# Performance work log

Hardware: AMD Instinct MI355X
Metric: run time of the kernel (lower is better)

Reference implementation:

```python
import jax, jax.numpy as jnp
import numpy as np

A_CUBIC = -0.75  # torch grid_sample bicubic convolution coefficient
INTERP_FACTOR = 0.25
WINDOW = 20
STEP = 4


def _cubic_interp_1d(signal):
    # Replicates torch bicubic grid_sample (align_corners=True, border padding)
    # on a (B,1,1,n) tensor, which reduces to 1D cubic convolution (A=-0.75).
    B, n = signal.shape
    num_points = int((n - 1) / INTERP_FACTOR) + 1
    pos = jnp.linspace(0.0, n - 1, num_points)  # sample positions in index space
    i0 = jnp.floor(pos).astype(jnp.int32)
    s = (pos - i0).astype(signal.dtype)  # frac in [0,1)
    A = A_CUBIC
    def w_far(d):   # 1 <= d <= 2
        return ((A * d - 5 * A) * d + 8 * A) * d - 4 * A
    def w_near(d):  # 0 <= d <= 1
        return ((A + 2) * d - (A + 3)) * d * d + 1
    w = jnp.stack([w_far(s + 1), w_near(s), w_near(1 - s), w_far(2 - s)], axis=-1)  # (P,4)
    idx = jnp.clip(i0[:, None] + jnp.arange(-1, 3)[None, :], 0, n - 1)  # border pad, (P,4)
    vals = signal[:, idx]  # (B,P,4)
    return jnp.einsum('bpk,pk->bp', vals, w)


def _apply_kernels(x, gamma_raw):
    # per-row shift so min >= 0 (only if min < 0), then softmax-weighted kernel mix
    m = jnp.min(x, axis=1, keepdims=True)
    x = x - jnp.minimum(m, 0.0)
    gamma = jax.nn.softmax(gamma_raw)
    poly = (x + 1.3) ** 2                      # polynomial: degree=2, offset=1.3
    gauss = jnp.exp(-0.5 * (x - 0.7) ** 2)     # gaussian: center=0.7, sigma=1.0
    return gamma[0] * poly + gamma[1] * gauss


def setup_inputs() -> dict:
    key = jax.random.key(0)
    return {
        'signal': jax.random.normal(key, (4, 1000), dtype=jnp.float32),
        'alpha': jnp.float32(0.15),
        'beta': jnp.float32(0.9),
        'gamma_raw': jnp.array([0.5, 0.5], dtype=jnp.float32),
    }


def reference(signal, alpha, beta, gamma_raw):
    interp = _cubic_interp_1d(signal)              # (B, n)
    ks = _apply_kernels(interp, gamma_raw)         # (B, n)
    B, n = ks.shape
    n_windows = (n - WINDOW) // STEP + 1
    starts = jnp.arange(n_windows) * STEP          # (W,)
    posn = jnp.arange(n)                           # (n,)
    in_win = (posn[None, :] >= starts[:, None]) & (posn[None, :] < starts[:, None] + WINDOW)
    in_win = in_win.astype(ks.dtype)               # (W, n)
    sig = ks[:, None, :]                           # (B,1,n)
    # M: fft of zero-padded window; M1: fft of signal with window zeroed out
    M = jnp.abs(jnp.fft.fft(sig * in_win[None], axis=-1))          # (B,W,n)
    M1 = jnp.abs(jnp.fft.fft(sig * (1.0 - in_win)[None], axis=-1))  # (B,W,n)
    x_max = jnp.max(M, axis=-1, keepdims=True)
    strong = (M > x_max * alpha).astype(M.dtype)
    combined = M1 * M * strong
    result = jnp.minimum(M, combined)              # (B,W,n)
    thr = beta * jnp.max(result.reshape(B, -1), axis=1)[:, None, None]
    result = result * (result > thr).astype(result.dtype)
    return result
```

## Files before the change

kernel.cpp:

```cpp
#include <hip/hip_runtime.h>
#include <math.h>

#define NSIG 1000
#define NP   3997
#define KHALF 1999
#define NW   995
#define WIN  20
#define STEPW 4
#define BATCH 4
#define NCH  125
#define CW   8


__device__ __forceinline__ double interp_at(const float* __restrict__ s, int p) {
    int i0 = p >> 2;
    int si = p & 3;
    double ss = 0.25 * (double)si;
    const double A = -0.75;
    double d0 = ss + 1.0;
    double w0 = ((A * d0 - 5.0 * A) * d0 + 8.0 * A) * d0 - 4.0 * A;
    double w1 = ((A + 2.0) * ss - (A + 3.0)) * ss * ss + 1.0;
    double d2 = 1.0 - ss;
    double w2 = ((A + 2.0) * d2 - (A + 3.0)) * d2 * d2 + 1.0;
    double d3 = 2.0 - ss;
    double w3 = ((A * d3 - 5.0 * A) * d3 + 8.0 * A) * d3 - 4.0 * A;
    int im1 = i0 - 1; if (im1 < 0) im1 = 0;
    int ip1 = i0 + 1; if (ip1 > NSIG - 1) ip1 = NSIG - 1;
    int ip2 = i0 + 2; if (ip2 > NSIG - 1) ip2 = NSIG - 1;
    return w0 * (double)s[im1] + w1 * (double)s[i0] +
           w2 * (double)s[ip1] + w3 * (double)s[ip2];
}

__global__ __launch_bounds__(512) void dft_init_kernel(
        const float* __restrict__ sig, const float* __restrict__ gamma_raw,
        float* __restrict__ ks, float2* __restrict__ tw, float2* __restrict__ S,
        unsigned int* __restrict__ rmax) {
    __shared__ float   lks[NP];
    __shared__ double2 redd[512];
    __shared__ double  rrs[16], ris[16];
    int b = blockIdx.y;
    int bx = blockIdx.x;
    int tid = threadIdx.x;
    const float* srow = sig + b * NSIG;
    const double TWO_PI = 6.283185307179586476925286766559;
    const double abase = -TWO_PI / (double)NP;

    double lmin = 1e300;
    #pragma unroll
    for (int i = 0; i < 8; ++i) {
        int p = tid + i * 512;
        if (p < NP) lmin = fmin(lmin, interp_at(srow, p));
    }
    redd[tid].x = lmin;
    __syncthreads();
    for (int s = 256; s > 0; s >>= 1) {
        if (tid < s) redd[tid].x = fmin(redd[tid].x, redd[tid + s].x);
        __syncthreads();
    }
    double m = fmin(redd[0].x, 0.0);
    double g0r = (double)gamma_raw[0], g1r = (double)gamma_raw[1];
    double mx = fmax(g0r, g1r);
    double e0 = exp(g0r - mx), e1 = exp(g1r - mx);
    double inv = 1.0 / (e0 + e1);
    double g0 = e0 * inv, g1 = e1 * inv;
    #pragma unroll
    for (int i = 0; i < 8; ++i) {
        int p = tid + i * 512;
        if (p < NP) {
            double x = interp_at(srow, p) - m;
            double poly = (x + 1.3) * (x + 1.3);
            double gauss = exp(-0.5 * (x - 0.7) * (x - 0.7));
            float v = (float)(g0 * poly + g1 * gauss);
            lks[p] = v;
            if (bx == 0) ks[b * NP + p] = v;
        }
    }
    if (b == 0 && bx < 8) {
        int mm = bx * 512 + tid;
        if (mm < NP) {
            double ang = abase * (double)mm;
            double sv, cv; sincos(ang, &sv, &cv);
            tw[mm] = make_float2((float)cv, (float)sv);
        }
        if (bx == 0 && tid < BATCH) rmax[tid] = 0u;
    }
    if (tid < 16) {
        double sv, cv;
        sincos(abase * (double)(bx * 16 + tid), &sv, &cv);
        rrs[tid] = cv; ris[tid] = sv;
    }
    __syncthreads();

    int kk = tid & 15, tc = tid >> 4;
    int k = bx * 16 + kk;
    double sr = 0.0, si = 0.0;
    if (k < KHALF) {
        int t0 = tc * 125;
        int t1 = t0 + 125; if (t1 > NP) t1 = NP;
        double rr = rrs[kk], ri = ris[kk];
        int m0 = (k * t0) % NP;
        double pr, pi;
        sincos(abase * (double)m0, &pi, &pr);
        for (int t = t0; t < t1; ++t) {
            double kv = (double)lks[t];
            sr = fma(kv, pr, sr);
            si = fma(kv, pi, si);
            double nr = pr * rr - pi * ri;
            double ni = pr * ri + pi * rr;
            pr = nr; pi = ni;
        }
    }
    redd[tid] = make_double2(sr, si);
    __syncthreads();
    for (int s = 256; s >= 16; s >>= 1) {
        if (tid < s) {
            redd[tid].x += redd[tid + s].x;
            redd[tid].y += redd[tid + s].y;
        }
        __syncthreads();
    }
    if (tid < 16) {
        int kw = bx * 16 + tid;
        if (kw < KHALF)
            S[b * NP + kw] = make_float2((float)redd[tid].x, (float)redd[tid].y);
    }
}

__device__ __forceinline__ float wavemax(float x) {
    #pragma unroll
    for (int off = 32; off > 0; off >>= 1)
        x = fmaxf(x, __shfl_xor(x, off));
    return x;
}

#define SLIDE1(n, co, cn) { \
    float ax = fmaf((cn), T##n.x, -(co)); \
    float ay = (cn) * T##n.y; \
    Wx##n = fmaf(ax, Q##n.x, fmaf(-ay, Q##n.y, Wx##n)); \
    Wy##n = fmaf(ax, Q##n.y, fmaf(ay, Q##n.x, Wy##n)); \
    float tq = fmaf(Q##n.x, R##n.x, -(Q##n.y * R##n.y)); \
    Q##n.y = fmaf(Q##n.x, R##n.y, Q##n.y * R##n.x); \
    Q##n.x = tq; }

#define SLIDEJ(co, cn) SLIDE1(0, co, cn) SLIDE1(1, co, cn) SLIDE1(2, co, cn) SLIDE1(3, co, cn)

#define SLIDE4(base) { \
    { float co = kp[(base) + 0], cn = kp[(base) + 20]; SLIDEJ(co, cn) } \
    { float co = kp[(base) + 1], cn = kp[(base) + 21]; SLIDEJ(co, cn) } \
    { float co = kp[(base) + 2], cn = kp[(base) + 22]; SLIDEJ(co, cn) } \
    { float co = kp[(base) + 3], cn = kp[(base) + 23]; SLIDEJ(co, cn) } }

#define SNAP() { Ax0=Wx0;Ay0=Wy0;Ax1=Wx1;Ay1=Wy1;Ax2=Wx2;Ay2=Wy2;Ax3=Wx3;Ay3=Wy3; }

#define MAX8(a) fmaxf(fmaxf(fmaxf((a)[0],(a)[1]),fmaxf((a)[2],(a)[3])), \
                      fmaxf(fmaxf((a)[4],(a)[5]),fmaxf((a)[6],(a)[7])))

#define PB(wa, bf) { \
    float MA0 = sqrtf(fmaf(Ax0,Ax0,Ay0*Ay0)); \
    float MA1 = sqrtf(fmaf(Ax1,Ax1,Ay1*Ay1)); \
    float MA2 = sqrtf(fmaf(Ax2,Ax2,Ay2*Ay2)); \
    float MA3 = sqrtf(fmaf(Ax3,Ax3,Ay3*Ay3)); \
    float MB0 = sqrtf(fmaf(Wx0,Wx0,Wy0*Wy0)); \
    float MB1 = sqrtf(fmaf(Wx1,Wx1,Wy1*Wy1)); \
    float MB2 = sqrtf(fmaf(Wx2,Wx2,Wy2*Wy2)); \
    float MB3 = sqrtf(fmaf(Wx3,Wx3,Wy3*Wy3)); \
    float lmA = fmaxf(fmaxf(MA0, MA1), fmaxf(MA2, v3 ? MA3 : 0.f)); \
    float lmB = fmaxf(fmaxf(MB0, MB1), fmaxf(MB2, v3 ? MB3 : 0.f)); \
    lmA = wavemax(lmA); \
    lmB = wavemax(lmB); \
    if ((tid & 63) == 0) { wrA[bf][wv] = lmA; wrB[bf][wv] = lmB; } \
    __syncthreads(); \
    float cutA = alpha * MAX8(wrA[bf]); \
    float cutB = alpha * MAX8(wrB[bf]); \
    if (w0 + (wa) < NW) { \
        if (tid == 0) wcut[b * NW + w0 + (wa)] = cutA; \
        float r0=0.f,r1=0.f,r2=0.f,r3=0.f; \
        { float dr=Sv0.x-Ax0, di=Sv0.y-Ay0; float m1=sqrtf(fmaf(dr,dr,di*di)); if (MA0>cutA) r0=fminf(MA0,m1*MA0); } \
        { float dr=Sv1.x-Ax1, di=Sv1.y-Ay1; float m1=sqrtf(fmaf(dr,dr,di*di)); if (MA1>cutA) r1=fminf(MA1,m1*MA1); } \
        { float dr=Sv2.x-Ax2, di=Sv2.y-Ay2; float m1=sqrtf(fmaf(dr,dr,di*di)); if (MA2>cutA) r2=fminf(MA2,m1*MA2); } \
        if (v3) { float dr=Sv3.x-Ax3, di=Sv3.y-Ay3; float m1=sqrtf(fmaf(dr,dr,di*di)); if (MA3>cutA) r3=fminf(MA3,m1*MA3); } \
        rl = fmaxf(rl, fmaxf(fmaxf(r0,r1),fmaxf(r2,r3))); \
    } \
    if (w0 + (wa) + 1 < NW) { \
        if (tid == 0) wcut[b * NW + w0 + (wa) + 1] = cutB; \
        float r0=0.f,r1=0.f,r2=0.f,r3=0.f; \
        { float dr=Sv0.x-Wx0, di=Sv0.y-Wy0; float m1=sqrtf(fmaf(dr,dr,di*di)); if (MB0>cutB) r0=fminf(MB0,m1*MB0); } \
        { float dr=Sv1.x-Wx1, di=Sv1.y-Wy1; float m1=sqrtf(fmaf(dr,dr,di*di)); if (MB1>cutB) r1=fminf(MB1,m1*MB1); } \
        { float dr=Sv2.x-Wx2, di=Sv2.y-Wy2; float m1=sqrtf(fmaf(dr,dr,di*di)); if (MB2>cutB) r2=fminf(MB2,m1*MB2); } \
        if (v3) { float dr=Sv3.x-Wx3, di=Sv3.y-Wy3; float m1=sqrtf(fmaf(dr,dr,di*di)); if (MB3>cutB) r3=fminf(MB3,m1*MB3); } \
        rl = fmaxf(rl, fmaxf(fmaxf(r0,r1),fmaxf(r2,r3))); \
    } }

__global__ __launch_bounds__(512, 4) void window_kernel(
        const float* __restrict__ ks, const float2* __restrict__ tw,
        const float2* __restrict__ S, const float* __restrict__ alpha_p,
        float* __restrict__ wcut, float* __restrict__ cmax,
        unsigned int* __restrict__ rmax) {
    __shared__ float wrA[2][8], wrB[2][8];
    int b = blockIdx.y;
    int wc = blockIdx.x;
    int w0 = wc * CW;
    int s0 = w0 * STEPW;
    int tid = threadIdx.x;
    int wv = tid >> 6;
    float alpha = *alpha_p;
    const float* kp = ks + b * NP + s0;

    int k0 = tid, k1 = tid + 512, k2 = tid + 1024, k3 = tid + 1536;
    bool v3 = (k3 < KHALF);

    float2 R0 = tw[k0], R1 = tw[k1], R2 = tw[k2], R3 = tw[k3];
    float2 T0 = tw[(20 * k0) % NP], T1 = tw[(20 * k1) % NP],
           T2 = tw[(20 * k2) % NP], T3 = tw[(20 * k3) % NP];
    float2 Q0 = tw[(k0 * s0) % NP], Q1 = tw[(k1 * s0) % NP],
           Q2 = tw[(k2 * s0) % NP], Q3 = tw[(k3 * s0) % NP];
    const float2* Sb = S + b * NP;
    float2 Sv0 = Sb[k0], Sv1 = Sb[k1], Sv2 = Sb[k2], Sv3 = Sb[k3];

    float Dx0 = kp[19], Dy0 = 0.f, Dx1 = kp[19], Dy1 = 0.f,
          Dx2 = kp[19], Dy2 = 0.f, Dx3 = kp[19], Dy3 = 0.f;
    #pragma unroll
    for (int j = 18; j >= 0; --j) {
        float a = kp[j];
        float nx, ny;
        nx = fmaf(Dx0, R0.x, fmaf(-Dy0, R0.y, a));
        ny = fmaf(Dy0, R0.x, Dx0 * R0.y);
        Dx0 = nx; Dy0 = ny;
        nx = fmaf(Dx1, R1.x, fmaf(-Dy1, R1.y, a));
        ny = fmaf(Dy1, R1.x, Dx1 * R1.y);
        Dx1 = nx; Dy1 = ny;
        nx = fmaf(Dx2, R2.x, fmaf(-Dy2, R2.y, a));
        ny = fmaf(Dy2, R2.x, Dx2 * R2.y);
        Dx2 = nx; Dy2 = ny;
        nx = fmaf(Dx3, R3.x, fmaf(-Dy3, R3.y, a));
        ny = fmaf(Dy3, R3.x, Dx3 * R3.y);
        Dx3 = nx; Dy3 = ny;
    }
    float Wx0 = fmaf(Q0.x, Dx0, -(Q0.y * Dy0));
    float Wy0 = fmaf(Q0.x, Dy0, Q0.y * Dx0);
    float Wx1 = fmaf(Q1.x, Dx1, -(Q1.y * Dy1));
    float Wy1 = fmaf(Q1.x, Dy1, Q1.y * Dx1);
    float Wx2 = fmaf(Q2.x, Dx2, -(Q2.y * Dy2));
    float Wy2 = fmaf(Q2.x, Dy2, Q2.y * Dx2);
    float Wx3 = fmaf(Q3.x, Dx3, -(Q3.y * Dy3));
    float Wy3 = fmaf(Q3.x, Dy3, Q3.y * Dx3);

    float Ax0, Ay0, Ax1, Ay1, Ax2, Ay2, Ax3, Ay3;
    float rl = 0.f;

    SNAP() SLIDE4(0)                    PB(0, 0)
    SLIDE4(4)  SNAP() SLIDE4(8)        PB(2, 1)
    SLIDE4(12) SNAP() SLIDE4(16)       PB(4, 0)
    SLIDE4(20) SNAP() SLIDE4(24)       PB(6, 1)

    rl = wavemax(rl);
    if ((tid & 63) == 0) wrA[0][wv] = rl;
    __syncthreads();
    if (tid == 0) {
        float bm = MAX8(wrA[0]);
        cmax[b * NCH + wc] = bm;
        atomicMax(&rmax[b], __float_as_uint(bm));
    }
}

#define FINBIN(n, kn, valid) { \
    if (valid) { \
        float M = sqrtf(fmaf(Dx##n, Dx##n, Dy##n * Dy##n)); \
        float2 P = tw[((kn) * start) % NP]; \
        float Wr = fmaf(P.x, Dx##n, -(P.y * Dy##n)); \
        float Wi = fmaf(P.x, Dy##n, P.y * Dx##n); \
        float2 Sv = Sb[kn]; \
        float dr = Sv.x - Wr, di = Sv.y - Wi; \
        float M1 = sqrtf(fmaf(dr, dr, di * di)); \
        float res = 0.f; \
        if (M > cut) res = fminf(M, M1 * M); \
        float f = (res > thr) ? res : 0.f; \
        out[base + (kn)] = f; \
        if ((kn) > 0) out[base + NP - (kn)] = f; \
    } }

__global__ __launch_bounds__(512) void finalize_kernel(
        const float* __restrict__ ks, const float2* __restrict__ tw,
        const float2* __restrict__ S, const float* __restrict__ wcut,
        const float* __restrict__ cmax, const unsigned int* __restrict__ rmax,
        const float* __restrict__ beta_p, float* __restrict__ out) {
    int b = blockIdx.y, w = blockIdx.x;
    int tid = threadIdx.x;
    float thr = (*beta_p) * __uint_as_float(rmax[b]);
    size_t base = (size_t)(b * NW + w) * NP;
    if (cmax[b * NCH + (w >> 3)] <= thr) {
        int h = ((4 - (int)(base & 3)) & 3);
        int nv = (NP - h) >> 2;
        int t0 = h + (nv << 2);
        float4* vp = (float4*)(out + base + h);
        float4 z4 = make_float4(0.f, 0.f, 0.f, 0.f);
        for (int v = tid; v < nv; v += 512) vp[v] = z4;
        if (tid < h) out[base + tid] = 0.f;
        if (tid < NP - t0) out[base + t0 + tid] = 0.f;
        return;
    }
    int start = w * STEPW;
    const float* kp = ks + b * NP + start;
    float cut = wcut[b * NW + w];
    const float2* Sb = S + b * NP;
    int k0 = tid, k1 = tid + 512, k2 = tid + 1024, k3 = tid + 1536;
    bool v3 = (k3 < KHALF);
    float2 R0 = tw[k0], R1 = tw[k1], R2 = tw[k2], R3 = tw[k3];
    float Dx0 = kp[19], Dy0 = 0.f, Dx1 = kp[19], Dy1 = 0.f,
          Dx2 = kp[19], Dy2 = 0.f, Dx3 = kp[19], Dy3 = 0.f;
    #pragma unroll
    for (int j = 18; j >= 0; --j) {
        float a = kp[j];
        float nx, ny;
        nx = fmaf(Dx0, R0.x, fmaf(-Dy0, R0.y, a));
        ny = fmaf(Dy0, R0.x, Dx0 * R0.y);
        Dx0 = nx; Dy0 = ny;
        nx = fmaf(Dx1, R1.x, fmaf(-Dy1, R1.y, a));
        ny = fmaf(Dy1, R1.x, Dx1 * R1.y);
        Dx1 = nx; Dy1 = ny;
        nx = fmaf(Dx2, R2.x, fmaf(-Dy2, R2.y, a));
        ny = fmaf(Dy2, R2.x, Dx2 * R2.y);
        Dx2 = nx; Dy2 = ny;
        nx = fmaf(Dx3, R3.x, fmaf(-Dy3, R3.y, a));
        ny = fmaf(Dy3, R3.x, Dx3 * R3.y);
        Dx3 = nx; Dy3 = ny;
    }
    FINBIN(0, k0, true)
    FINBIN(1, k1, true)
    FINBIN(2, k2, true)
    FINBIN(3, k3, v3)
}

extern "C" void kernel_launch(void* const* d_in, const int* in_sizes, int n_in,
                              void* d_out, int out_size, void* d_ws, size_t ws_size,
                              hipStream_t stream) {
    const float* sig       = (const float*)d_in[0];
    const float* alpha_p   = (const float*)d_in[1];
    const float* beta_p    = (const float*)d_in[2];
    const float* gamma_raw = (const float*)d_in[3];
    char* ws = (char*)d_ws;
    float*        ks   = (float*)(ws + 0);
    float2*       tw   = (float2*)(ws + 65536);
    float2*       S    = (float2*)(ws + 98304);
    unsigned int* rmax = (unsigned int*)(ws + 226304);
    float*        cmax = (float*)(ws + 226432);
    float*        wcut = (float*)(ws + 229376);
    float* out = (float*)d_out;

    hipLaunchKernelGGL(dft_init_kernel, dim3(125, BATCH), dim3(512), 0, stream,
                       sig, gamma_raw, ks, tw, S, rmax);
    hipLaunchKernelGGL(window_kernel,   dim3(NCH, BATCH), dim3(512), 0, stream,
                       ks, tw, S, alpha_p, wcut, cmax, rmax);
    hipLaunchKernelGGL(finalize_kernel, dim3(NW, BATCH),  dim3(512), 0, stream,
                       ks, tw, S, wcut, cmax, rmax, beta_p, out);
}
```

Measured before the change: 58.16 us.

## Zero-fill output inside window kernel, make finalize sparse per chunk

```diff
diff --git a/kernel.cpp b/kernel.cpp
--- a/kernel.cpp
+++ b/kernel.cpp
@@ -154,6 +154,15 @@
 
 #define MAX8(a) fmaxf(fmaxf(fmaxf((a)[0],(a)[1]),fmaxf((a)[2],(a)[3])), \
                       fmaxf(fmaxf((a)[4],(a)[5]),fmaxf((a)[6],(a)[7])))
+
+#define ZSLOT(c) { \
+    int vlo = (c) * zper; \
+    int vhi = vlo + zper; if (vhi > znv) vhi = znv; \
+    for (int v = vlo + tid; v < vhi; v += 512) zvp[v] = z4; \
+    if ((c) == 0) { \
+        if (tid < zh) out[zbase + tid] = 0.f; \
+        if (tid < zt) out[zbase + zhv + tid] = 0.f; \
+    } }
 
 #define PB(wa, bf) { \
     float MA0 = sqrtf(fmaf(Ax0,Ax0,Ay0*Ay0)); \
@@ -195,7 +204,7 @@
         const float* __restrict__ ks, const float2* __restrict__ tw,
         const float2* __restrict__ S, const float* __restrict__ alpha_p,
         float* __restrict__ wcut, float* __restrict__ cmax,
-        unsigned int* __restrict__ rmax) {
+        unsigned int* __restrict__ rmax, float* __restrict__ out) {
     __shared__ float wrA[2][8], wrB[2][8];
     int b = blockIdx.y;
     int wc = blockIdx.x;
@@ -216,6 +225,19 @@
            Q2 = tw[(k2 * s0) % NP], Q3 = tw[(k3 * s0) % NP];
     const float2* Sb = S + b * NP;
     float2 Sv0 = Sb[k0], Sv1 = Sb[k1], Sv2 = Sb[k2], Sv3 = Sb[k3];
+
+    size_t zbase = (size_t)(b * NW + w0) * NP;
+    int znrows = NW - w0; if (znrows > CW) znrows = CW;
+    size_t znflt = (size_t)znrows * NP;
+    int zh = (4 - (int)(zbase & 3)) & 3;
+    int znv = (int)((znflt - (size_t)zh) >> 2);
+    int zhv = zh + (znv << 2);
+    int zt = (int)(znflt - (size_t)zhv);
+    int zper = (znv + 4) / 5;
+    float4* zvp = (float4*)(out + zbase + zh);
+    float4 z4 = make_float4(0.f, 0.f, 0.f, 0.f);
+
+    ZSLOT(0)
 
     float Dx0 = kp[19], Dy0 = 0.f, Dx1 = kp[19], Dy1 = 0.f,
           Dx2 = kp[19], Dy2 = 0.f, Dx3 = kp[19], Dy3 = 0.f;
@@ -249,9 +271,13 @@
     float rl = 0.f;
 
     SNAP() SLIDE4(0)                    PB(0, 0)
+    ZSLOT(1)
     SLIDE4(4)  SNAP() SLIDE4(8)        PB(2, 1)
+    ZSLOT(2)
     SLIDE4(12) SNAP() SLIDE4(16)       PB(4, 0)
+    ZSLOT(3)
     SLIDE4(20) SNAP() SLIDE4(24)       PB(6, 1)
+    ZSLOT(4)
 
     rl = wavemax(rl);
     if ((tid & 63) == 0) wrA[0][wv] = rl;
@@ -279,56 +305,52 @@
         if ((kn) > 0) out[base + NP - (kn)] = f; \
     } }
 
-__global__ __launch_bounds__(512) void finalize_kernel(
+__global__ __launch_bounds__(512) void sparse_kernel(
         const float* __restrict__ ks, const float2* __restrict__ tw,
         const float2* __restrict__ S, const float* __restrict__ wcut,
         const float* __restrict__ cmax, const unsigned int* __restrict__ rmax,
         const float* __restrict__ beta_p, float* __restrict__ out) {
-    int b = blockIdx.y, w = blockIdx.x;
+    int b = blockIdx.y, wc = blockIdx.x;
+    float thr = (*beta_p) * __uint_as_float(rmax[b]);
+    if (cmax[b * NCH + wc] <= thr) return;
+
     int tid = threadIdx.x;
-    float thr = (*beta_p) * __uint_as_float(rmax[b]);
-    size_t base = (size_t)(b * NW + w) * NP;
-    if (cmax[b * NCH + (w >> 3)] <= thr) {
-        int h = ((4 - (int)(base & 3)) & 3);
-        int nv = (NP - h) >> 2;
-        int t0 = h + (nv << 2);
-        float4* vp = (float4*)(out + base + h);
-        float4 z4 = make_float4(0.f, 0.f, 0.f, 0.f);
-        for (int v = tid; v < nv; v += 512) vp[v] = z4;
-        if (tid < h) out[base + tid] = 0.f;
-        if (tid < NP - t0) out[base + t0 + tid] = 0.f;
-        return;
-    }
-    int start = w * STEPW;
-    const float* kp = ks + b * NP + start;
-    float cut = wcut[b * NW + w];
-    const float2* Sb = S + b * NP;
     int k0 = tid, k1 = tid + 512, k2 = tid + 1024, k3 = tid + 1536;
     bool v3 = (k3 < KHALF);
     float2 R0 = tw[k0], R1 = tw[k1], R2 = tw[k2], R3 = tw[k3];
-    float Dx0 = kp[19], Dy0 = 0.f, Dx1 = kp[19], Dy1 = 0.f,
-          Dx2 = kp[19], Dy2 = 0.f, Dx3 = kp[19], Dy3 = 0.f;
-    #pragma unroll
-    for (int j = 18; j >= 0; --j) {
-        float a = kp[j];
-        float nx, ny;
-        nx = fmaf(Dx0, R0.x, fmaf(-Dy0, R0.y, a));
-        ny = fmaf(Dy0, R0.x, Dx0 * R0.y);
-        Dx0 = nx; Dy0 = ny;
-        nx = fmaf(Dx1, R1.x, fmaf(-Dy1, R1.y, a));
-        ny = fmaf(Dy1, R1.x, Dx1 * R1.y);
-        Dx1 = nx; Dy1 = ny;
-        nx = fmaf(Dx2, R2.x, fmaf(-Dy2, R2.y, a));
-        ny = fmaf(Dy2, R2.x, Dx2 * R2.y);
-        Dx2 = nx; Dy2 = ny;
-        nx = fmaf(Dx3, R3.x, fmaf(-Dy3, R3.y, a));
-        ny = fmaf(Dy3, R3.x, Dx3 * R3.y);
-        Dx3 = nx; Dy3 = ny;
-    }
-    FINBIN(0, k0, true)
-    FINBIN(1, k1, true)
-    FINBIN(2, k2, true)
-    FINBIN(3, k3, v3)
+    const float2* Sb = S + b * NP;
+
+    for (int i = 0; i < CW; ++i) {
+        int w = wc * CW + i;
+        if (w >= NW) break;
+        int start = w * STEPW;
+        const float* kp = ks + b * NP + start;
+        float cut = wcut[b * NW + w];
+        size_t base = (size_t)(b * NW + w) * NP;
+        float Dx0 = kp[19], Dy0 = 0.f, Dx1 = kp[19], Dy1 = 0.f,
+              Dx2 = kp[19], Dy2 = 0.f, Dx3 = kp[19], Dy3 = 0.f;
+        #pragma unroll
+        for (int j = 18; j >= 0; --j) {
+            float a = kp[j];
+            float nx, ny;
+            nx = fmaf(Dx0, R0.x, fmaf(-Dy0, R0.y, a));
+            ny = fmaf(Dy0, R0.x, Dx0 * R0.y);
+            Dx0 = nx; Dy0 = ny;
+            nx = fmaf(Dx1, R1.x, fmaf(-Dy1, R1.y, a));
+            ny = fmaf(Dy1, R1.x, Dx1 * R1.y);
+            Dx1 = nx; Dy1 = ny;
+            nx = fmaf(Dx2, R2.x, fmaf(-Dy2, R2.y, a));
+            ny = fmaf(Dy2, R2.x, Dx2 * R2.y);
+            Dx2 = nx; Dy2 = ny;
+            nx = fmaf(Dx3, R3.x, fmaf(-Dy3, R3.y, a));
+            ny = fmaf(Dy3, R3.x, Dx3 * R3.y);
+            Dx3 = nx; Dy3 = ny;
+        }
+        FINBIN(0, k0, true)
+        FINBIN(1, k1, true)
+        FINBIN(2, k2, true)
+        FINBIN(3, k3, v3)
+    }
 }
 
 extern "C" void kernel_launch(void* const* d_in, const int* in_sizes, int n_in,
@@ -350,7 +372,7 @@
     hipLaunchKernelGGL(dft_init_kernel, dim3(125, BATCH), dim3(512), 0, stream,
                        sig, gamma_raw, ks, tw, S, rmax);
     hipLaunchKernelGGL(window_kernel,   dim3(NCH, BATCH), dim3(512), 0, stream,
-                       ks, tw, S, alpha_p, wcut, cmax, rmax);
-    hipLaunchKernelGGL(finalize_kernel, dim3(NW, BATCH),  dim3(512), 0, stream,
+                       ks, tw, S, alpha_p, wcut, cmax, rmax, out);
+    hipLaunchKernelGGL(sparse_kernel,   dim3(NCH, BATCH), dim3(512), 0, stream,
                        ks, tw, S, wcut, cmax, rmax, beta_p, out);
 }
```

Measured after the change: 75.90 us. +30.5%, slower.

## Pair windows per finalize block and split DFT twiddle recurrence into two chains

Applied to the files above, without the earlier changes.

```diff
diff --git a/kernel.cpp b/kernel.cpp
--- a/kernel.cpp
+++ b/kernel.cpp
@@ -10,6 +10,7 @@
 #define BATCH 4
 #define NCH  125
 #define CW   8
+#define NR2  498
 
 
 __device__ __forceinline__ double interp_at(const float* __restrict__ s, int p) {
@@ -98,17 +99,35 @@
         int t0 = tc * 125;
         int t1 = t0 + 125; if (t1 > NP) t1 = NP;
         double rr = rrs[kk], ri = ris[kk];
+        double rr2 = rr * rr - ri * ri;
+        double ri2 = 2.0 * rr * ri;
         int m0 = (k * t0) % NP;
-        double pr, pi;
-        sincos(abase * (double)m0, &pi, &pr);
-        for (int t = t0; t < t1; ++t) {
+        double p0r, p0i;
+        sincos(abase * (double)m0, &p0i, &p0r);
+        double p1r = p0r * rr - p0i * ri;
+        double p1i = p0r * ri + p0i * rr;
+        double s2r = 0.0, s2i = 0.0;
+        int t = t0;
+        for (; t + 1 < t1; t += 2) {
+            double k0v = (double)lks[t];
+            double k1v = (double)lks[t + 1];
+            sr  = fma(k0v, p0r, sr);
+            si  = fma(k0v, p0i, si);
+            s2r = fma(k1v, p1r, s2r);
+            s2i = fma(k1v, p1i, s2i);
+            double n0r = p0r * rr2 - p0i * ri2;
+            double n0i = p0r * ri2 + p0i * rr2;
+            p0r = n0r; p0i = n0i;
+            double n1r = p1r * rr2 - p1i * ri2;
+            double n1i = p1r * ri2 + p1i * rr2;
+            p1r = n1r; p1i = n1i;
+        }
+        if (t < t1) {
             double kv = (double)lks[t];
-            sr = fma(kv, pr, sr);
-            si = fma(kv, pi, si);
-            double nr = pr * rr - pi * ri;
-            double ni = pr * ri + pi * rr;
-            pr = nr; pi = ni;
+            sr = fma(kv, p0r, sr);
+            si = fma(kv, p0i, si);
         }
+        sr += s2r; si += s2i;
     }
     redd[tid] = make_double2(sr, si);
     __syncthreads();
@@ -263,51 +282,19 @@
     }
 }
 
-#define FINBIN(n, kn, valid) { \
-    if (valid) { \
-        float M = sqrtf(fmaf(Dx##n, Dx##n, Dy##n * Dy##n)); \
-        float2 P = tw[((kn) * start) % NP]; \
-        float Wr = fmaf(P.x, Dx##n, -(P.y * Dy##n)); \
-        float Wi = fmaf(P.x, Dy##n, P.y * Dx##n); \
-        float2 Sv = Sb[kn]; \
-        float dr = Sv.x - Wr, di = Sv.y - Wi; \
-        float M1 = sqrtf(fmaf(dr, dr, di * di)); \
-        float res = 0.f; \
-        if (M > cut) res = fminf(M, M1 * M); \
-        float f = (res > thr) ? res : 0.f; \
-        out[base + (kn)] = f; \
-        if ((kn) > 0) out[base + NP - (kn)] = f; \
-    } }
-
-__global__ __launch_bounds__(512) void finalize_kernel(
+__device__ __forceinline__ void survivor_row(
         const float* __restrict__ ks, const float2* __restrict__ tw,
-        const float2* __restrict__ S, const float* __restrict__ wcut,
-        const float* __restrict__ cmax, const unsigned int* __restrict__ rmax,
-        const float* __restrict__ beta_p, float* __restrict__ out) {
-    int b = blockIdx.y, w = blockIdx.x;
-    int tid = threadIdx.x;
-    float thr = (*beta_p) * __uint_as_float(rmax[b]);
-    size_t base = (size_t)(b * NW + w) * NP;
-    if (cmax[b * NCH + (w >> 3)] <= thr) {
-        int h = ((4 - (int)(base & 3)) & 3);
-        int nv = (NP - h) >> 2;
-        int t0 = h + (nv << 2);
-        float4* vp = (float4*)(out + base + h);
-        float4 z4 = make_float4(0.f, 0.f, 0.f, 0.f);
-        for (int v = tid; v < nv; v += 512) vp[v] = z4;
-        if (tid < h) out[base + tid] = 0.f;
-        if (tid < NP - t0) out[base + t0 + tid] = 0.f;
-        return;
-    }
+        const float2* __restrict__ Sb, const float* __restrict__ wcut,
+        float* __restrict__ out, int b, int w, float thr, int tid) {
     int start = w * STEPW;
     const float* kp = ks + b * NP + start;
     float cut = wcut[b * NW + w];
-    const float2* Sb = S + b * NP;
-    int k0 = tid, k1 = tid + 512, k2 = tid + 1024, k3 = tid + 1536;
-    bool v3 = (k3 < KHALF);
-    float2 R0 = tw[k0], R1 = tw[k1], R2 = tw[k2], R3 = tw[k3];
-    float Dx0 = kp[19], Dy0 = 0.f, Dx1 = kp[19], Dy1 = 0.f,
-          Dx2 = kp[19], Dy2 = 0.f, Dx3 = kp[19], Dy3 = 0.f;
+    size_t base = (size_t)(b * NW + w) * NP;
+    int k0 = tid, k1 = tid + 1024;
+    bool v1 = (k1 < KHALF);
+    int k1c = v1 ? k1 : 0;
+    float2 R0 = tw[k0], R1 = tw[k1c];
+    float Dx0 = kp[19], Dy0 = 0.f, Dx1 = kp[19], Dy1 = 0.f;
     #pragma unroll
     for (int j = 18; j >= 0; --j) {
         float a = kp[j];
@@ -318,17 +305,75 @@
         nx = fmaf(Dx1, R1.x, fmaf(-Dy1, R1.y, a));
         ny = fmaf(Dy1, R1.x, Dx1 * R1.y);
         Dx1 = nx; Dy1 = ny;
-        nx = fmaf(Dx2, R2.x, fmaf(-Dy2, R2.y, a));
-        ny = fmaf(Dy2, R2.x, Dx2 * R2.y);
-        Dx2 = nx; Dy2 = ny;
-        nx = fmaf(Dx3, R3.x, fmaf(-Dy3, R3.y, a));
-        ny = fmaf(Dy3, R3.x, Dx3 * R3.y);
-        Dx3 = nx; Dy3 = ny;
-    }
-    FINBIN(0, k0, true)
-    FINBIN(1, k1, true)
-    FINBIN(2, k2, true)
-    FINBIN(3, k3, v3)
+    }
+    {
+        float M = sqrtf(fmaf(Dx0, Dx0, Dy0 * Dy0));
+        float2 P = tw[(k0 * start) % NP];
+        float Wr = fmaf(P.x, Dx0, -(P.y * Dy0));
+        float Wi = fmaf(P.x, Dy0, P.y * Dx0);
+        float2 Sv = Sb[k0];
+        float dr = Sv.x - Wr, di = Sv.y - Wi;
+        float M1 = sqrtf(fmaf(dr, dr, di * di));
+        float res = 0.f;
+        if (M > cut) res = fminf(M, M1 * M);
+        float f = (res > thr) ? res : 0.f;
+        out[base + k0] = f;
+        if (k0 > 0) out[base + NP - k0] = f;
+    }
+    if (v1) {
+        float M = sqrtf(fmaf(Dx1, Dx1, Dy1 * Dy1));
+        float2 P = tw[(k1 * start) % NP];
+        float Wr = fmaf(P.x, Dx1, -(P.y * Dy1));
+        float Wi = fmaf(P.x, Dy1, P.y * Dx1);
+        float2 Sv = Sb[k1];
+        float dr = Sv.x - Wr, di = Sv.y - Wi;
+        float M1 = sqrtf(fmaf(dr, dr, di * di));
+        float res = 0.f;
+        if (M > cut) res = fminf(M, M1 * M);
+        float f = (res > thr) ? res : 0.f;
+        out[base + k1] = f;
+        out[base + NP - k1] = f;
+    }
+}
+
+__device__ __forceinline__ void zero_span(float* __restrict__ out, size_t base,
+                                          size_t nflt, int tid) {
+    int h = (4 - (int)(base & 3)) & 3;
+    size_t nv = (nflt - (size_t)h) >> 2;
+    size_t t0 = (size_t)h + (nv << 2);
+    float4* vp = (float4*)(out + base + h);
+    float4 z4 = make_float4(0.f, 0.f, 0.f, 0.f);
+    for (size_t v = tid; v < nv; v += 1024) vp[v] = z4;
+    if (tid < h) out[base + tid] = 0.f;
+    if ((size_t)tid < nflt - t0) out[base + t0 + tid] = 0.f;
+}
+
+__global__ __launch_bounds__(1024) void finalize_kernel(
+        const float* __restrict__ ks, const float2* __restrict__ tw,
+        const float2* __restrict__ S, const float* __restrict__ wcut,
+        const float* __restrict__ cmax, const unsigned int* __restrict__ rmax,
+        const float* __restrict__ beta_p, float* __restrict__ out) {
+    int b = blockIdx.y;
+    int w0 = blockIdx.x * 2;
+    int w1 = w0 + 1;
+    bool have1 = (w1 < NW);
+    int tid = threadIdx.x;
+    float thr = (*beta_p) * __uint_as_float(rmax[b]);
+    bool dead0 = (cmax[b * NCH + (w0 >> 3)] <= thr);
+    bool dead1 = !have1 || (cmax[b * NCH + (w1 >> 3)] <= thr);
+    size_t base0 = (size_t)(b * NW + w0) * NP;
+
+    if (dead0 && dead1) {
+        zero_span(out, base0, (size_t)(have1 ? 2 : 1) * NP, tid);
+        return;
+    }
+    const float2* Sb = S + b * NP;
+    if (dead0) zero_span(out, base0, NP, tid);
+    else       survivor_row(ks, tw, Sb, wcut, out, b, w0, thr, tid);
+    if (have1) {
+        if (dead1) zero_span(out, base0 + NP, NP, tid);
+        else       survivor_row(ks, tw, Sb, wcut, out, b, w1, thr, tid);
+    }
 }
 
 extern "C" void kernel_launch(void* const* d_in, const int* in_sizes, int n_in,
@@ -347,10 +392,10 @@
     float*        wcut = (float*)(ws + 229376);
     float* out = (float*)d_out;
 
-    hipLaunchKernelGGL(dft_init_kernel, dim3(125, BATCH), dim3(512), 0, stream,
+    hipLaunchKernelGGL(dft_init_kernel, dim3(125, BATCH), dim3(512),  0, stream,
                        sig, gamma_raw, ks, tw, S, rmax);
-    hipLaunchKernelGGL(window_kernel,   dim3(NCH, BATCH), dim3(512), 0, stream,
+    hipLaunchKernelGGL(window_kernel,   dim3(NCH, BATCH), dim3(512),  0, stream,
                        ks, tw, S, alpha_p, wcut, cmax, rmax);
-    hipLaunchKernelGGL(finalize_kernel, dim3(NW, BATCH),  dim3(512), 0, stream,
+    hipLaunchKernelGGL(finalize_kernel, dim3(NR2, BATCH), dim3(1024), 0, stream,
                        ks, tw, S, wcut, cmax, rmax, beta_p, out);
 }
```

Result: no change. 58.81 us (+1.1%).
